# Optimization experiments

Measured on AMD Instinct MI355X. Metric: run time of the kernel, lower is better.

## Reference

```python
import jax, jax.numpy as jnp
import numpy as np

P = 2.0            # power-mean exponent (init kwarg p)
NUM_NODES = 1_000_000
D_FEAT = 128
NUM_GRAPHS = 4096


def setup_inputs() -> dict:
    key = jax.random.key(0)
    kx, kb = jax.random.split(key)
    x = jax.random.normal(kx, (NUM_NODES, D_FEAT), dtype=jnp.float32)
    batch = jnp.sort(jax.random.randint(kb, (NUM_NODES,), 0, NUM_GRAPHS, dtype=jnp.int64))
    return {"x": x, "batch": batch}


def reference(x, batch):
    # x: [N, D] node features; batch: [N] sorted graph ids in [0, NUM_GRAPHS)
    xp = x ** P                                                   # elementwise pow
    seg_sum = jax.ops.segment_sum(xp, batch, num_segments=NUM_GRAPHS)  # [G, D]
    counts = jax.ops.segment_sum(jnp.ones((x.shape[0],), dtype=x.dtype), batch,
                                 num_segments=NUM_GRAPHS)         # [G]
    # scatter_mean semantics: empty segments yield 0 (clamp count to avoid 0/0)
    mean = seg_sum / jnp.maximum(counts, 1.0)[:, None]            # [G, D]
    return mean ** (1.0 / P)
```

## Files before the change

### kernel.cpp

```cpp
#include <hip/hip_runtime.h>
#include <math.h>


#define D_FEAT 128
#define DV (D_FEAT / 4)

__global__ __launch_bounds__(256) void seg_offsets_kernel(
    const int* __restrict__ batch, int* __restrict__ off, int N, int G)
{
    int i = blockIdx.x * blockDim.x + threadIdx.x;
    if (i >= N) return;
    int cur = batch[i];
    if (i == 0) {
        for (int g = 0; g <= cur; ++g) off[g] = 0;
    } else {
        int prev = batch[i - 1];
        for (int g = prev + 1; g <= cur; ++g) off[g] = i;
    }
    if (i == N - 1) {
        for (int g = cur + 1; g <= G; ++g) off[g] = N;
    }
}

__global__ __launch_bounds__(256) void global_powermean_pooling_44126493999223_kernel(
    const float* __restrict__ x,
    const int* __restrict__ off,
    float* __restrict__ out)
{
    const int g    = blockIdx.x;
    const int tid  = threadIdx.x;
    const int fg   = tid & 31;
    const int lane = tid >> 5;

    const int start = off[g];
    const int end   = off[g + 1];
    const int count = end - start;

    const float4* __restrict__ x4 = (const float4*)x;

    float4 a0 = make_float4(0.f, 0.f, 0.f, 0.f);
    float4 a1 = a0, a2 = a0, a3 = a0;

    int r = start + lane;
    for (; r + 24 < end; r += 32) {
        float4 v0 = x4[(size_t)(r     ) * DV + fg];
        float4 v1 = x4[(size_t)(r +  8) * DV + fg];
        float4 v2 = x4[(size_t)(r + 16) * DV + fg];
        float4 v3 = x4[(size_t)(r + 24) * DV + fg];
        a0.x += v0.x * v0.x; a0.y += v0.y * v0.y; a0.z += v0.z * v0.z; a0.w += v0.w * v0.w;
        a1.x += v1.x * v1.x; a1.y += v1.y * v1.y; a1.z += v1.z * v1.z; a1.w += v1.w * v1.w;
        a2.x += v2.x * v2.x; a2.y += v2.y * v2.y; a2.z += v2.z * v2.z; a2.w += v2.w * v2.w;
        a3.x += v3.x * v3.x; a3.y += v3.y * v3.y; a3.z += v3.z * v3.z; a3.w += v3.w * v3.w;
    }
    for (; r < end; r += 8) {
        float4 v = x4[(size_t)r * DV + fg];
        a0.x += v.x * v.x; a0.y += v.y * v.y; a0.z += v.z * v.z; a0.w += v.w * v.w;
    }
    a0.x += a1.x + a2.x + a3.x;
    a0.y += a1.y + a2.y + a3.y;
    a0.z += a1.z + a2.z + a3.z;
    a0.w += a1.w + a2.w + a3.w;

    __shared__ float4 red[256];
    red[tid] = a0;
    __syncthreads();
    for (int o = 4; o >= 1; o >>= 1) {
        if (lane < o) {
            float4 a = red[tid];
            float4 b = red[tid + o * 32];
            a.x += b.x; a.y += b.y; a.z += b.z; a.w += b.w;
            red[tid] = a;
        }
        __syncthreads();
    }

    if (lane == 0) {
        const float inv = 1.0f / (float)(count > 0 ? count : 1);
        float4 s = red[tid];
        float4 o;
        o.x = sqrtf(s.x * inv);
        o.y = sqrtf(s.y * inv);
        o.z = sqrtf(s.z * inv);
        o.w = sqrtf(s.w * inv);
        ((float4*)out)[(size_t)g * DV + fg] = o;
    }
}

extern "C" void kernel_launch(void* const* d_in, const int* in_sizes, int n_in,
                              void* d_out, int out_size, void* d_ws, size_t ws_size,
                              hipStream_t stream) {
    const float* x     = (const float*)d_in[0];
    const int*   batch = (const int*)d_in[1];
    float*       out   = (float*)d_out;

    const int N = in_sizes[1];
    const int G = out_size / D_FEAT;

    int* off = (int*)d_ws;

    seg_offsets_kernel<<<(N + 255) / 256, 256, 0, stream>>>(batch, off, N, G);
    global_powermean_pooling_44126493999223_kernel<<<G, 256, 0, stream>>>(x, off, out);
}
```

Measured before the change: 650.2 us.

## Split each segment across blocks with atomics and binary-search segment bounds

Replaces the per-node offsets kernel with a binary search over the sorted batch array inside each block. Each graph segment is now split across four blocks that accumulate partial squared sums into the output with atomicAdd, and a separate finalize kernel applies the mean and sqrt. Loads become nontemporal and launch bounds request higher occupancy. The aim is more parallelism and less offset-building overhead, at the cost of an extra zeroing kernel, a finalize kernel, atomics, and a nondeterministic summation order.

```diff
diff --git a/kernel.cpp b/kernel.cpp
--- a/kernel.cpp
+++ b/kernel.cpp
@@ -4,86 +4,103 @@
 
 #define D_FEAT 128
 #define DV (D_FEAT / 4)
+#define SPLIT 4
 
-__global__ __launch_bounds__(256) void seg_offsets_kernel(
-    const int* __restrict__ batch, int* __restrict__ off, int N, int G)
+typedef float f32x4 __attribute__((ext_vector_type(4)));
+
+__global__ __launch_bounds__(256) void zero_out_kernel(f32x4* __restrict__ out4, int n4)
 {
-    int i = blockIdx.x * blockDim.x + threadIdx.x;
-    if (i >= N) return;
-    int cur = batch[i];
-    if (i == 0) {
-        for (int g = 0; g <= cur; ++g) off[g] = 0;
-    } else {
-        int prev = batch[i - 1];
-        for (int g = prev + 1; g <= cur; ++g) off[g] = i;
-    }
-    if (i == N - 1) {
-        for (int g = cur + 1; g <= G; ++g) off[g] = N;
-    }
+    int i = blockIdx.x * 256 + threadIdx.x;
+    if (i < n4) out4[i] = (f32x4)0.f;
 }
 
-__global__ __launch_bounds__(256) void global_powermean_pooling_44126493999223_kernel(
-    const float* __restrict__ x,
-    const int* __restrict__ off,
-    float* __restrict__ out)
+__global__ __launch_bounds__(256, 8) void global_powermean_pooling_44126493999223_kernel(
+    const f32x4* __restrict__ x4,
+    const int*   __restrict__ batch,
+    float*       __restrict__ out,
+    int N)
 {
-    const int g    = blockIdx.x;
+    const int g    = blockIdx.x >> 2;
+    const int s    = blockIdx.x & (SPLIT - 1);
     const int tid  = threadIdx.x;
     const int fg   = tid & 31;
     const int lane = tid >> 5;
 
-    const int start = off[g];
-    const int end   = off[g + 1];
-    const int count = end - start;
+    __shared__ int sb[2];
+    if (tid == 0 || tid == 64) {
+        const int target = g + (tid >> 6);
+        int lo = 0, hi = N;
+        while (lo < hi) {
+            int mid = (lo + hi) >> 1;
+            if (batch[mid] < target) lo = mid + 1; else hi = mid;
+        }
+        sb[tid >> 6] = lo;
+    }
+    __syncthreads();
+    const int start = sb[0];
+    const int cnt   = sb[1] - start;
+    const int rs = start + (cnt * s) / SPLIT;
+    const int re = start + (cnt * (s + 1)) / SPLIT;
 
-    const float4* __restrict__ x4 = (const float4*)x;
+    f32x4 a0 = (f32x4)0.f, a1 = (f32x4)0.f, a2 = (f32x4)0.f, a3 = (f32x4)0.f;
 
-    float4 a0 = make_float4(0.f, 0.f, 0.f, 0.f);
-    float4 a1 = a0, a2 = a0, a3 = a0;
+    int r = rs + lane;
+    const f32x4* __restrict__ p = x4 + (size_t)r * DV + fg;
+    for (; r + 24 < re; r += 32, p += 32 * DV) {
+        f32x4 v0 = __builtin_nontemporal_load(p);
+        f32x4 v1 = __builtin_nontemporal_load(p +  8 * DV);
+        f32x4 v2 = __builtin_nontemporal_load(p + 16 * DV);
+        f32x4 v3 = __builtin_nontemporal_load(p + 24 * DV);
+        a0 += v0 * v0;
+        a1 += v1 * v1;
+        a2 += v2 * v2;
+        a3 += v3 * v3;
+    }
+    for (; r < re; r += 8, p += 8 * DV) {
+        f32x4 v = __builtin_nontemporal_load(p);
+        a0 += v * v;
+    }
+    a0 += a1; a2 += a3; a0 += a2;
 
-    int r = start + lane;
-    for (; r + 24 < end; r += 32) {
-        float4 v0 = x4[(size_t)(r     ) * DV + fg];
-        float4 v1 = x4[(size_t)(r +  8) * DV + fg];
-        float4 v2 = x4[(size_t)(r + 16) * DV + fg];
-        float4 v3 = x4[(size_t)(r + 24) * DV + fg];
-        a0.x += v0.x * v0.x; a0.y += v0.y * v0.y; a0.z += v0.z * v0.z; a0.w += v0.w * v0.w;
-        a1.x += v1.x * v1.x; a1.y += v1.y * v1.y; a1.z += v1.z * v1.z; a1.w += v1.w * v1.w;
-        a2.x += v2.x * v2.x; a2.y += v2.y * v2.y; a2.z += v2.z * v2.z; a2.w += v2.w * v2.w;
-        a3.x += v3.x * v3.x; a3.y += v3.y * v3.y; a3.z += v3.z * v3.z; a3.w += v3.w * v3.w;
-    }
-    for (; r < end; r += 8) {
-        float4 v = x4[(size_t)r * DV + fg];
-        a0.x += v.x * v.x; a0.y += v.y * v.y; a0.z += v.z * v.z; a0.w += v.w * v.w;
-    }
-    a0.x += a1.x + a2.x + a3.x;
-    a0.y += a1.y + a2.y + a3.y;
-    a0.z += a1.z + a2.z + a3.z;
-    a0.w += a1.w + a2.w + a3.w;
-
-    __shared__ float4 red[256];
+    __shared__ f32x4 red[256];
     red[tid] = a0;
     __syncthreads();
-    for (int o = 4; o >= 1; o >>= 1) {
-        if (lane < o) {
-            float4 a = red[tid];
-            float4 b = red[tid + o * 32];
-            a.x += b.x; a.y += b.y; a.z += b.z; a.w += b.w;
-            red[tid] = a;
+    if (lane < 4) red[tid] += red[tid + 128];
+    __syncthreads();
+    if (lane < 2) red[tid] += red[tid + 64];
+    __syncthreads();
+    if (lane == 0) {
+        f32x4 ssum = red[tid] + red[tid + 32];
+        float* dst = out + (size_t)g * D_FEAT + fg * 4;
+        atomicAdd(dst + 0, ssum[0]);
+        atomicAdd(dst + 1, ssum[1]);
+        atomicAdd(dst + 2, ssum[2]);
+        atomicAdd(dst + 3, ssum[3]);
+    }
+}
+
+__global__ __launch_bounds__(128) void finalize_kernel(
+    const int* __restrict__ batch, float* __restrict__ out, int N)
+{
+    const int g = blockIdx.x;
+    const int d = threadIdx.x;
+
+    __shared__ int sb[2];
+    if (d == 0 || d == 64) {
+        const int target = g + (d >> 6);
+        int lo = 0, hi = N;
+        while (lo < hi) {
+            int mid = (lo + hi) >> 1;
+            if (batch[mid] < target) lo = mid + 1; else hi = mid;
         }
-        __syncthreads();
+        sb[d >> 6] = lo;
     }
+    __syncthreads();
+    const int cnt = sb[1] - sb[0];
 
-    if (lane == 0) {
-        const float inv = 1.0f / (float)(count > 0 ? count : 1);
-        float4 s = red[tid];
-        float4 o;
-        o.x = sqrtf(s.x * inv);
-        o.y = sqrtf(s.y * inv);
-        o.z = sqrtf(s.z * inv);
-        o.w = sqrtf(s.w * inv);
-        ((float4*)out)[(size_t)g * DV + fg] = o;
-    }
+    const size_t i = (size_t)g * D_FEAT + d;
+    const float v = out[i];
+    out[i] = (cnt > 0) ? sqrtf(v / (float)cnt) : 0.f;
 }
 
 extern "C" void kernel_launch(void* const* d_in, const int* in_sizes, int n_in,
@@ -96,8 +113,9 @@
     const int N = in_sizes[1];
     const int G = out_size / D_FEAT;
 
-    int* off = (int*)d_ws;
-
-    seg_offsets_kernel<<<(N + 255) / 256, 256, 0, stream>>>(batch, off, N, G);
-    global_powermean_pooling_44126493999223_kernel<<<G, 256, 0, stream>>>(x, off, out);
+    const int n4 = G * DV;
+    zero_out_kernel<<<(n4 + 255) / 256, 256, 0, stream>>>((f32x4*)out, n4);
+    global_powermean_pooling_44126493999223_kernel
+        <<<G * SPLIT, 256, 0, stream>>>((const f32x4*)x, batch, out, N);
+    finalize_kernel<<<G, 128, 0, stream>>>(batch, out, N);
 }
```

New measurement: 673.8 us. 3.6% more time.
